# Optimization experiments

Hardware: AMD Instinct MI355X
Metric: run time of the kernel (lower is better)

The kernel has to match this reference:

```python
import jax, jax.numpy as jnp
import numpy as np

INV_L_MIN, INV_L_MAX = 0.5, 2.0

def _gelu(x):
    return jax.nn.gelu(x, approximate=False)

def _scaled_sigmoid(x, lo, hi):
    return lo + (hi - lo) * jax.nn.sigmoid(x)

def _fourier_bases(nodes, modes):
    # nodes: [b, n, d]; modes: [k, d, w] -> temp: [b, n, k, w]
    temp = 2.0 * jnp.pi * jnp.einsum('bxd,kdw->bxkw', nodes, modes)
    return jnp.cos(temp), jnp.sin(temp), jnp.ones_like(temp[:, :, :1, :])

def _spectral_conv(x, wc, ws, w0, bc, bs, b0, wbc, wbs, wb0):
    # x: [b, c_in, n]; forward non-uniform Fourier transform via weighted bases
    x_c = jnp.einsum('bix,bxkw->bikw', x, wbc)
    x_s = -jnp.einsum('bix,bxkw->bikw', x, wbs)
    x_0 = jnp.einsum('bix,bxkw->bikw', x, wb0)
    f_c = jnp.einsum('bikw,iokw->bokw', x_c, wc) - jnp.einsum('bikw,iokw->bokw', x_s, ws)
    f_s = jnp.einsum('bikw,iokw->bokw', x_s, wc) + jnp.einsum('bikw,iokw->bokw', x_c, ws)
    f_0 = jnp.einsum('bikw,iokw->bokw', x_0, w0)
    return (jnp.einsum('bokw,bxkw->box', f_0, b0)
            + 2.0 * jnp.einsum('bokw,bxkw->box', f_c, bc)
            - 2.0 * jnp.einsum('bokw,bxkw->box', f_s, bs))


def setup_inputs() -> dict:
    key = jax.random.key(0)
    ks = jax.random.split(key, 32)
    B, NU, NV = 4, 65536, 16384
    K, D, W = 32, 2, 1          # nmodes, ndims, nmeasures
    C, L = 64, 3                # channels, number of BNO layers
    FC, IU, IV, OUT = 128, 2, 3, 1
    f32 = jnp.float32
    rn = lambda k, s, sc=1.0: (sc * jax.random.normal(k, s, dtype=f32))
    ru = lambda k, s, sc=1.0: (sc * jax.random.uniform(k, s, dtype=f32))
    sp_scale = 1.0 / (C * C)
    inp = {
        'u': rn(ks[0], (B, NU, IU)),
        'v': rn(ks[1], (B, NV, IV)),
        'node_mask_u': jnp.ones((B, NU, 1), dtype=jnp.int32),
        'nodes_u': ru(ks[2], (B, NU, D)),
        'nodes_v': ru(ks[3], (B, NV, D)),
        'node_weights_u': ru(ks[4], (B, NU, W), 1.0 / NU),
        'node_weights_v': ru(ks[5], (B, NV, W), 1.0 / NV),
        'modes': ru(ks[6], (K, D, W), 8.0),
        # scaled_logit(1.0, 0.5, 2.0) = log((1-0.5)/(2-1)) = log(0.5)
        'inv_L_scale_latent': jnp.full((D, W), -0.69314718, dtype=f32),
        'fc0_u_w': rn(ks[7], (C, IU), 0.5), 'fc0_u_b': rn(ks[8], (C,), 0.1),
        'fc0_v_w': rn(ks[9], (C, IV), 0.5), 'fc0_v_b': rn(ks[10], (C,), 0.1),
        'sp_ext_wc': ru(ks[11], (L, C, C, K, W), sp_scale),
        'sp_ext_ws': ru(ks[12], (L, C, C, K, W), sp_scale),
        'sp_ext_w0': ru(ks[13], (L, C, C, 1, W), sp_scale),
        'sp_u_wc': ru(ks[14], (L, C, C, K, W), sp_scale),
        'sp_u_ws': ru(ks[15], (L, C, C, K, W), sp_scale),
        'sp_u_w0': ru(ks[16], (L, C, C, 1, W), sp_scale),
        'sp_v_wc': ru(ks[17], (L, C, C, K, W), sp_scale),
        'sp_v_ws': ru(ks[18], (L, C, C, K, W), sp_scale),
        'sp_v_w0': ru(ks[19], (L, C, C, 1, W), sp_scale),
        'ws_u_w': rn(ks[20], (L, C, C), 0.05), 'ws_u_b': rn(ks[21], (L, C), 0.02),
        'ws_v_w': rn(ks[22], (L, C, C), 0.05), 'ws_v_b': rn(ks[23], (L, C), 0.02),
        'fc1_w': rn(ks[24], (FC, C), 0.05), 'fc1_b': rn(ks[25], (FC,), 0.02),
        'fc2_w': rn(ks[26], (OUT, FC), 0.05), 'fc2_b': rn(ks[27], (OUT,), 0.02),
    }
    return inp


def reference(u, v, node_mask_u, nodes_u, nodes_v, node_weights_u, node_weights_v,
              modes, inv_L_scale_latent, fc0_u_w, fc0_u_b, fc0_v_w, fc0_v_b,
              sp_ext_wc, sp_ext_ws, sp_ext_w0, sp_u_wc, sp_u_ws, sp_u_w0,
              sp_v_wc, sp_v_ws, sp_v_w0, ws_u_w, ws_u_b, ws_v_w, ws_v_b,
              fc1_w, fc1_b, fc2_w, fc2_b):
    # node_mask_u is unpacked but unused in the original forward
    m = modes * _scaled_sigmoid(inv_L_scale_latent, INV_L_MIN, INV_L_MAX)  # [k,d,w]
    bc_u, bs_u, b0_u = _fourier_bases(nodes_u, m)
    bc_v, bs_v, b0_v = _fourier_bases(nodes_v, m)
    wu = node_weights_u[:, :, None, :]  # [b,x,1,w]
    wv = node_weights_v[:, :, None, :]
    wbc_u, wbs_u, wb0_u = bc_u * wu, bs_u * wu, b0_u * wu
    wbc_v, wbs_v, wb0_v = bc_v * wv, bs_v * wv, b0_v * wv
    # lift to channel dim and move to [b, c, n]
    u = jnp.einsum('bxi,oi->box', u, fc0_u_w) + fc0_u_b[None, :, None]
    v = jnp.einsum('bxi,oi->box', v, fc0_v_w) + fc0_v_b[None, :, None]
    L = ws_u_w.shape[0]
    for i in range(L):
        u1 = _spectral_conv(v, sp_ext_wc[i], sp_ext_ws[i], sp_ext_w0[i],
                            bc_u, bs_u, b0_u, wbc_v, wbs_v, wb0_v)
        u2 = _spectral_conv(u, sp_u_wc[i], sp_u_ws[i], sp_u_w0[i],
                            bc_u, bs_u, b0_u, wbc_u, wbs_u, wb0_u)
        u3 = jnp.einsum('oi,bix->box', ws_u_w[i], u) + ws_u_b[i][None, :, None]
        u = u1 + u2 + u3
        if i != L - 1:  # v is only updated on non-final layers, as in the original
            u = _gelu(u)
            v1 = _spectral_conv(v, sp_v_wc[i], sp_v_ws[i], sp_v_w0[i],
                                bc_v, bs_v, b0_v, wbc_v, wbs_v, wb0_v)
            v2 = jnp.einsum('oi,bix->box', ws_v_w[i], v) + ws_v_b[i][None, :, None]
            v = _gelu(v1 + v2)
    u = jnp.transpose(u, (0, 2, 1))  # [b, n, c]
    u = _gelu(u @ fc1_w.T + fc1_b)
    return u @ fc2_w.T + fc2_b
```

## Files before the change

kernel.cpp:

```cpp
#include <hip/hip_runtime.h>
#include <math.h>

#define PI2 6.283185307179586f

typedef __attribute__((ext_vector_type(8))) short bf16x8;
typedef __attribute__((ext_vector_type(4))) float f32x4;

__device__ __forceinline__ float gelu_f(float x) {
    return 0.5f * x * (1.0f + erff(x * 0.7071067811865476f));
}
__device__ __forceinline__ unsigned short f2bf(float f) {
    unsigned int u = __float_as_uint(f);
    u += 0x7FFFu + ((u >> 16) & 1u);
    return (unsigned short)(u >> 16);
}
__device__ __forceinline__ float bf2f(unsigned short h) {
    return __uint_as_float(((unsigned int)h) << 16);
}
__device__ __forceinline__ unsigned int pk(unsigned short a, unsigned short b) {
    return (unsigned int)a | ((unsigned int)b << 16);
}
__device__ __forceinline__ void wsplit(float w, unsigned short* dst) {
    unsigned short h = f2bf(w);
    dst[0] = h;
    dst[128] = f2bf(w - bf2f(h));
}

template<int NIN>
__global__ __launch_bounds__(256) void k_prep(const float* __restrict__ nodes, const float* __restrict__ modes,
                                              const float* __restrict__ latent, const float* __restrict__ nw,
                                              const float* __restrict__ inp, const float* __restrict__ fcw,
                                              const float* __restrict__ fcb,
                                              unsigned short* __restrict__ FT, unsigned short* __restrict__ wbb,
                                              unsigned short* __restrict__ chbf, int N) {
    int b = blockIdx.y;
    int x = blockIdx.x * 256 + threadIdx.x;
    float s0 = 0.5f + 1.5f / (1.0f + expf(-latent[0]));
    float s1 = 0.5f + 1.5f / (1.0f + expf(-latent[1]));
    float n0 = nodes[((size_t)b * N + x) * 2 + 0];
    float n1 = nodes[((size_t)b * N + x) * 2 + 1];
    float wx = nw[(size_t)b * N + x];
    unsigned short* wb = wbb + (size_t)b * 65 * N + x;
    unsigned int row[64];
    #pragma unroll
    for (int k = 0; k < 32; ++k) {
        float m0 = modes[k * 2 + 0] * s0;
        float m1 = modes[k * 2 + 1] * s1;
        float t = PI2 * (n0 * m0 + n1 * m1);
        float s, c;
        sincosf(t, &s, &c);
        unsigned short hc = f2bf(c), hs = f2bf(s);
        if (k & 1) { row[k >> 1] |= ((unsigned int)hc << 16); row[16 + (k >> 1)] |= ((unsigned int)hs << 16); }
        else       { row[k >> 1] = hc;                         row[16 + (k >> 1)] = hs; }
        wb[(size_t)k * N] = f2bf(c * wx);
        wb[(size_t)(32 + k) * N] = f2bf(s * wx);
    }
    wb[(size_t)64 * N] = f2bf(wx);
    float xi[NIN];
    #pragma unroll
    for (int i = 0; i < NIN; ++i) xi[i] = inp[((size_t)b * N + x) * NIN + i];
    unsigned short* cb = chbf + (size_t)b * 64 * N + x;
    #pragma unroll
    for (int c = 0; c < 64; ++c) {
        float a = fcb[c];
        #pragma unroll
        for (int i = 0; i < NIN; ++i) a += fcw[c * NIN + i] * xi[i];
        unsigned short h = f2bf(a);
        cb[(size_t)c * N] = h;
        if (c & 1) row[32 + (c >> 1)] |= ((unsigned int)h << 16);
        else row[32 + (c >> 1)] = h;
    }
    unsigned int* fr = (unsigned int*)(FT + ((size_t)b * N + x) * 128);
    #pragma unroll
    for (int i = 0; i < 64; ++i) fr[i] = row[i];
}

__global__ __launch_bounds__(256) void k_analysis2(const unsigned short* __restrict__ chbf_u,
                                                   const unsigned short* __restrict__ wbb_u,
                                                   const unsigned short* __restrict__ chbf_v,
                                                   const unsigned short* __restrict__ wbb_v,
                                                   float* __restrict__ part_u, float* __restrict__ part_v,
                                                   int NU_, int NV_, int chu, int chv) {
    int b = blockIdx.y, bx = blockIdx.x, tid = threadIdx.x;
    const unsigned short *chb, *wb;
    float* pb;
    int N, xlen, chunk;
    if (bx < chu) {
        chunk = bx; N = NU_; xlen = NU_ / chu;
        chb = chbf_u + (size_t)b * 64 * N;
        wb = wbb_u + (size_t)b * 65 * N;
        pb = part_u + (size_t)(b * chu + chunk) * 64 * 66;
    } else {
        chunk = bx - chu; N = NV_; xlen = NV_ / chv;
        chb = chbf_v + (size_t)b * 64 * N;
        wb = wbb_v + (size_t)b * 65 * N;
        pb = part_v + (size_t)(b * chv + chunk) * 64 * 66;
    }
    int lane = tid & 63, wv = tid >> 6;
    int lm = lane & 15, lg = lane >> 4;
    int ro = wv * 16;
    int x0 = chunk * xlen;
    f32x4 acc[5] = {};
    for (int x = x0; x < x0 + xlen; x += 32) {
        bf16x8 a = *(const bf16x8*)(chb + (size_t)(ro + lm) * N + x + lg * 8);
        #pragma unroll
        for (int ct = 0; ct < 4; ++ct) {
            bf16x8 bf = *(const bf16x8*)(wb + (size_t)(ct * 16 + lm) * N + x + lg * 8);
            acc[ct] = __builtin_amdgcn_mfma_f32_16x16x32_bf16(a, bf, acc[ct], 0, 0, 0);
        }
        bf16x8 wf = *(const bf16x8*)(wb + (size_t)64 * N + x + lg * 8);
        acc[4] = __builtin_amdgcn_mfma_f32_16x16x32_bf16(a, wf, acc[4], 0, 0, 0);
    }
    #pragma unroll
    for (int ct = 0; ct < 4; ++ct)
        #pragma unroll
        for (int j = 0; j < 4; ++j)
            pb[(ro + lg * 4 + j) * 66 + ct * 16 + lm] = acc[ct][j];
    if (lm == 0) {
        #pragma unroll
        for (int j = 0; j < 4; ++j) pb[(ro + lg * 4 + j) * 66 + 64] = acc[4][j];
    }
}

__global__ void k_reduce2(const float* __restrict__ part_u, const float* __restrict__ part_v,
                          float* __restrict__ momu, float* __restrict__ momv, int chu, int chv, int B_) {
    int by = blockIdx.y;
    const float* p;
    float* m;
    int nch, b;
    if (by < B_) { b = by; p = part_u; m = momu; nch = chu; }
    else { b = by - B_; p = part_v; m = momv; nch = chv; }
    int e = blockIdx.x * 256 + threadIdx.x;
    if (e >= 64 * 65) return;
    int row = e / 65, col = e % 65;
    const float* pp = p + ((size_t)(b * nch) * 64 + row) * 66 + col;
    float s = 0.f;
    #pragma unroll 4
    for (int c = 0; c < nch; ++c)
        s += pp[(size_t)c * 64 * 66];
    m[((size_t)b * 64 + row) * 66 + col] = s;
}

__global__ __launch_bounds__(256) void k_tw(const float* __restrict__ e_c, const float* __restrict__ e_s,
                                            const float* __restrict__ u_c, const float* __restrict__ u_s,
                                            const float* __restrict__ v_c, const float* __restrict__ v_s,
                                            float* __restrict__ oT) {
    int li = blockIdx.x;
    int a = blockIdx.y;
    const float* in;
    switch (a) {
        case 0: in = e_c; break;
        case 1: in = e_s; break;
        case 2: in = u_c; break;
        case 3: in = u_s; break;
        case 4: in = v_c; break;
        default: in = v_s; break;
    }
    float* outp = oT + (size_t)a * 393216;
    int l = li >> 6, i = li & 63;
    __shared__ float t[32][65];
    int tid = threadIdx.x;
    const float* ib = in + (size_t)l * 131072 + (size_t)i * 2048;
    #pragma unroll
    for (int r = 0; r < 8; ++r) {
        int e = r * 256 + tid;
        t[e & 31][e >> 5] = ib[e];
    }
    __syncthreads();
    float* ob = outp + (size_t)l * 131072 + (size_t)i * 64;
    #pragma unroll
    for (int r = 0; r < 8; ++r) {
        int e = r * 256 + tid;
        ob[(size_t)(e >> 6) * 4096 + (e & 63)] = t[e >> 6][e & 63];
    }
}

__global__ void k_buildW(const float* __restrict__ momu, const float* __restrict__ momv,
                         const float* __restrict__ ecT, const float* __restrict__ esT, const float* __restrict__ ew0,
                         const float* __restrict__ ucT, const float* __restrict__ usT, const float* __restrict__ uw0,
                         const float* __restrict__ vcT, const float* __restrict__ vsT, const float* __restrict__ vw0,
                         const float* __restrict__ wsuw, const float* __restrict__ wsub,
                         const float* __restrict__ wsvw, const float* __restrict__ wsvb,
                         unsigned short* __restrict__ WuBf, unsigned short* __restrict__ WvBf,
                         float* __restrict__ biasU, float* __restrict__ biasV, int do_v) {
    int b = blockIdx.y, j = blockIdx.x, o = threadIdx.x;
    const float* mu = momu + (size_t)b * 64 * 66;
    const float* mv = momv + (size_t)b * 64 * 66;
    unsigned short* Wub = WuBf + ((size_t)b * 64 + o) * 256;
    unsigned short* Wvb = WvBf + ((size_t)b * 64 + o) * 256;
    if (j < 32) {
        int k = j;
        const float* ec = ecT + (size_t)k * 4096;
        const float* es = esT + (size_t)k * 4096;
        const float* uc = ucT + (size_t)k * 4096;
        const float* us = usT + (size_t)k * 4096;
        const float* vc = vcT + (size_t)k * 4096;
        const float* vs = vsT + (size_t)k * 4096;
        float fcu = 0, fsu = 0, fcv = 0, fsv = 0;
        for (int i = 0; i < 64; ++i) {
            float Scv = mv[i * 66 + k], Ssv = mv[i * 66 + 32 + k];
            float Scu = mu[i * 66 + k], Ssu = mu[i * 66 + 32 + k];
            int wi = i * 64 + o;
            float e_c = ec[wi], e_s = es[wi];
            float u_c = uc[wi], u_s = us[wi];
            fcu += Scv * e_c + Ssv * e_s + Scu * u_c + Ssu * u_s;
            fsu += Scv * e_s - Ssv * e_c + Scu * u_s - Ssu * u_c;
            if (do_v) {
                float v_c = vc[wi], v_s = vs[wi];
                fcv += Scv * v_c + Ssv * v_s;
                fsv += Scv * v_s - Ssv * v_c;
            }
        }
        wsplit(2.f * fcu, Wub + k);
        wsplit(-2.f * fsu, Wub + 32 + k);
        if (do_v) {
            wsplit(2.f * fcv, Wvb + k);
            wsplit(-2.f * fsv, Wvb + 32 + k);
        }
    } else {
        for (int c = 0; c < 64; ++c) wsplit(wsuw[o * 64 + c], Wub + 64 + c);
        float f0u = 0;
        for (int i = 0; i < 64; ++i)
            f0u += mv[i * 66 + 64] * ew0[i * 64 + o] + mu[i * 66 + 64] * uw0[i * 64 + o];
        biasU[b * 64 + o] = f0u + wsub[o];
        if (do_v) {
            for (int c = 0; c < 64; ++c) wsplit(wsvw[o * 64 + c], Wvb + 64 + c);
            float f0v = 0;
            for (int i = 0; i < 64; ++i) f0v += mv[i * 66 + 64] * vw0[i * 64 + o];
            biasV[b * 64 + o] = f0v + wsvb[o];
        }
    }
}

__global__ void k_buildW_slow(const float* __restrict__ momu, const float* __restrict__ momv,
                              const float* __restrict__ ewc, const float* __restrict__ ews, const float* __restrict__ ew0,
                              const float* __restrict__ uwc, const float* __restrict__ uws, const float* __restrict__ uw0,
                              const float* __restrict__ vwc, const float* __restrict__ vws, const float* __restrict__ vw0,
                              const float* __restrict__ wsuw, const float* __restrict__ wsub,
                              const float* __restrict__ wsvw, const float* __restrict__ wsvb,
                              unsigned short* __restrict__ WuBf, unsigned short* __restrict__ WvBf,
                              float* __restrict__ biasU, float* __restrict__ biasV, int do_v) {
    int b = blockIdx.y, j = blockIdx.x, o = threadIdx.x;
    const float* mu = momu + (size_t)b * 64 * 66;
    const float* mv = momv + (size_t)b * 64 * 66;
    unsigned short* Wub = WuBf + ((size_t)b * 64 + o) * 256;
    unsigned short* Wvb = WvBf + ((size_t)b * 64 + o) * 256;
    if (j < 32) {
        int k = j;
        float fcu = 0, fsu = 0, fcv = 0, fsv = 0;
        for (int i = 0; i < 64; ++i) {
            float Scv = mv[i * 66 + k], Ssv = mv[i * 66 + 32 + k];
            float Scu = mu[i * 66 + k], Ssu = mu[i * 66 + 32 + k];
            int wi = (i * 64 + o) * 32 + k;
            float ec = ewc[wi], es = ews[wi];
            float uc = uwc[wi], us = uws[wi];
            fcu += Scv * ec + Ssv * es + Scu * uc + Ssu * us;
            fsu += Scv * es - Ssv * ec + Scu * us - Ssu * uc;
            if (do_v) {
                float vc = vwc[wi], vs = vws[wi];
                fcv += Scv * vc + Ssv * vs;
                fsv += Scv * vs - Ssv * vc;
            }
        }
        wsplit(2.f * fcu, Wub + k);
        wsplit(-2.f * fsu, Wub + 32 + k);
        if (do_v) {
            wsplit(2.f * fcv, Wvb + k);
            wsplit(-2.f * fsv, Wvb + 32 + k);
        }
    } else {
        for (int c = 0; c < 64; ++c) wsplit(wsuw[o * 64 + c], Wub + 64 + c);
        float f0u = 0;
        for (int i = 0; i < 64; ++i)
            f0u += mv[i * 66 + 64] * ew0[i * 64 + o] + mu[i * 66 + 64] * uw0[i * 64 + o];
        biasU[b * 64 + o] = f0u + wsub[o];
        if (do_v) {
            for (int c = 0; c < 64; ++c) wsplit(wsvw[o * 64 + c], Wvb + 64 + c);
            float f0v = 0;
            for (int i = 0; i < 64; ++i) f0v += mv[i * 66 + 64] * vw0[i * 64 + o];
            biasV[b * 64 + o] = f0v + wsvb[o];
        }
    }
}

__global__ __launch_bounds__(256) void k_synth3(const unsigned short* __restrict__ WuBf,
                                                const unsigned short* __restrict__ WvBf,
                                                const float* __restrict__ biasU, const float* __restrict__ biasV,
                                                unsigned short* FTu, unsigned short* FTv,
                                                const unsigned short* __restrict__ wbb_u,
                                                const unsigned short* __restrict__ wbb_v,
                                                float* __restrict__ part_u, float* __restrict__ part_v,
                                                int NU_, int NV_, int nbu, int act_u, int wft_v, int do_mom) {
    int bx = blockIdx.x, b = blockIdx.y, tid = threadIdx.x;
    const unsigned short* Wb;
    const float* bi;
    unsigned short* FT;
    const unsigned short* wb;
    float* pb;
    int N, act, wft, blk;
    if (bx < nbu) {
        blk = bx; Wb = WuBf; bi = biasU; FT = FTu; N = NU_;
        wb = wbb_u + (size_t)b * 65 * NU_;
        pb = part_u + (size_t)(b * (NU_ / 256) + blk) * 64 * 66;
        act = act_u; wft = 1;
    } else {
        blk = bx - nbu; Wb = WvBf; bi = biasV; FT = FTv; N = NV_;
        wb = wbb_v + (size_t)b * 65 * NV_;
        pb = part_v + (size_t)(b * (NV_ / 256) + blk) * 64 * 66;
        act = 1; wft = wft_v;
    }
    int lane = tid & 63, wv = tid >> 6;
    int lm = lane & 15, lg = lane >> 4;
    int ro = wv * 16;
    const unsigned short* Wrow = Wb + ((size_t)b * 64 + ro + lm) * 256;
    bf16x8 ahi[4], alo[4];
    #pragma unroll
    for (int kt = 0; kt < 4; ++kt) {
        ahi[kt] = *(const bf16x8*)(Wrow + kt * 32 + lg * 8);
        alo[kt] = *(const bf16x8*)(Wrow + 128 + kt * 32 + lg * 8);
    }
    float bias[4];
    #pragma unroll
    for (int j = 0; j < 4; ++j) bias[j] = bi[b * 64 + ro + lg * 4 + j];
    unsigned short* ftb = FT + (size_t)b * N * 128;
    __shared__ unsigned short st2[64][136];
    f32x4 macc[5] = {};
    int r0 = ro + lg * 4;
    for (int t = 0; t < 2; ++t) {
        int x0 = blk * 256 + t * 128;
        f32x4 acc[8] = {};
        #pragma unroll
        for (int xt = 0; xt < 8; ++xt) {
            int x = x0 + xt * 16 + lm;
            const unsigned short* fp = ftb + (size_t)x * 128 + lg * 8;
            #pragma unroll
            for (int kt = 0; kt < 4; ++kt) {
                bf16x8 bf = *(const bf16x8*)(fp + kt * 32);
                acc[xt] = __builtin_amdgcn_mfma_f32_16x16x32_bf16(ahi[kt], bf, acc[xt], 0, 0, 0);
                acc[xt] = __builtin_amdgcn_mfma_f32_16x16x32_bf16(alo[kt], bf, acc[xt], 0, 0, 0);
            }
        }
        __syncthreads();
        #pragma unroll
        for (int xt = 0; xt < 8; ++xt) {
            int xl = xt * 16 + lm;
            float v[4];
            #pragma unroll
            for (int j = 0; j < 4; ++j) {
                v[j] = acc[xt][j] + bias[j];
                if (act) v[j] = gelu_f(v[j]);
            }
            unsigned short h[4];
            #pragma unroll
            for (int j = 0; j < 4; ++j) h[j] = f2bf(v[j]);
            if (do_mom) {
                st2[r0 + 0][xl] = h[0];
                st2[r0 + 1][xl] = h[1];
                st2[r0 + 2][xl] = h[2];
                st2[r0 + 3][xl] = h[3];
            }
            if (wft) {
                unsigned int* dst = (unsigned int*)(ftb + (size_t)(x0 + xl) * 128 + 64 + r0);
                dst[0] = pk(h[0], h[1]);
                dst[1] = pk(h[2], h[3]);
            }
        }
        if (do_mom) {
            __syncthreads();
            #pragma unroll
            for (int xs = 0; xs < 128; xs += 32) {
                bf16x8 a = *(const bf16x8*)&st2[ro + lm][xs + lg * 8];
                #pragma unroll
                for (int ct = 0; ct < 4; ++ct) {
                    bf16x8 bw = *(const bf16x8*)(wb + (size_t)(ct * 16 + lm) * N + x0 + xs + lg * 8);
                    macc[ct] = __builtin_amdgcn_mfma_f32_16x16x32_bf16(a, bw, macc[ct], 0, 0, 0);
                }
                bf16x8 wf = *(const bf16x8*)(wb + (size_t)64 * N + x0 + xs + lg * 8);
                macc[4] = __builtin_amdgcn_mfma_f32_16x16x32_bf16(a, wf, macc[4], 0, 0, 0);
            }
        }
    }
    if (do_mom) {
        #pragma unroll
        for (int ct = 0; ct < 4; ++ct)
            #pragma unroll
            for (int j = 0; j < 4; ++j)
                pb[(r0 + j) * 66 + ct * 16 + lm] = macc[ct][j];
        if (lm == 0) {
            #pragma unroll
            for (int j = 0; j < 4; ++j) pb[(r0 + j) * 66 + 64] = macc[4][j];
        }
    }
}

__global__ __launch_bounds__(256) void k_fc12(const unsigned short* __restrict__ FT, const float* __restrict__ w1,
                                              const float* __restrict__ b1, const float* __restrict__ w2,
                                              const float* __restrict__ b2, float* __restrict__ out, int N) {
    int b = blockIdx.y, blk = blockIdx.x, tid = threadIdx.x;
    int lane = tid & 63, wv = tid >> 6;
    int lm = lane & 15, lg = lane >> 4;
    int f0 = wv * 32;
    bf16x8 ahi[2][2], alo[2][2];
    #pragma unroll
    for (int ft = 0; ft < 2; ++ft)
        #pragma unroll
        for (int kt = 0; kt < 2; ++kt) {
            const float* wp = w1 + (size_t)(f0 + ft * 16 + lm) * 64 + kt * 32 + lg * 8;
            float tmp[8];
            *(float4*)&tmp[0] = *(const float4*)wp;
            *(float4*)&tmp[4] = *(const float4*)(wp + 4);
            #pragma unroll
            for (int i = 0; i < 8; ++i) {
                unsigned short h = f2bf(tmp[i]);
                ahi[ft][kt][i] = (short)h;
                alo[ft][kt][i] = (short)f2bf(tmp[i] - bf2f(h));
            }
        }
    float b1v[2][4], w2v[2][4];
    #pragma unroll
    for (int ft = 0; ft < 2; ++ft)
        #pragma unroll
        for (int j = 0; j < 4; ++j) {
            int f = f0 + ft * 16 + lg * 4 + j;
            b1v[ft][j] = b1[f];
            w2v[ft][j] = w2[f];
        }
    f32x4 acc[8][2] = {};
    const unsigned short* ftb = FT + (size_t)b * N * 128;
    int x0 = blk * 128;
    #pragma unroll
    for (int xt = 0; xt < 8; ++xt) {
        const unsigned short* fp = ftb + (size_t)(x0 + xt * 16 + lm) * 128 + 64 + lg * 8;
        bf16x8 bf0 = *(const bf16x8*)fp;
        bf16x8 bf1 = *(const bf16x8*)(fp + 32);
        #pragma unroll
        for (int ft = 0; ft < 2; ++ft) {
            acc[xt][ft] = __builtin_amdgcn_mfma_f32_16x16x32_bf16(ahi[ft][0], bf0, acc[xt][ft], 0, 0, 0);
            acc[xt][ft] = __builtin_amdgcn_mfma_f32_16x16x32_bf16(alo[ft][0], bf0, acc[xt][ft], 0, 0, 0);
            acc[xt][ft] = __builtin_amdgcn_mfma_f32_16x16x32_bf16(ahi[ft][1], bf1, acc[xt][ft], 0, 0, 0);
            acc[xt][ft] = __builtin_amdgcn_mfma_f32_16x16x32_bf16(alo[ft][1], bf1, acc[xt][ft], 0, 0, 0);
        }
    }
    __shared__ float red[4][8][16];
    #pragma unroll
    for (int xt = 0; xt < 8; ++xt) {
        float s = 0.f;
        #pragma unroll
        for (int ft = 0; ft < 2; ++ft)
            #pragma unroll
            for (int j = 0; j < 4; ++j) {
                float v = acc[xt][ft][j] + b1v[ft][j];
                s += w2v[ft][j] * gelu_f(v);
            }
        s += __shfl_xor(s, 16, 64);
        s += __shfl_xor(s, 32, 64);
        if (lg == 0) red[wv][xt][lm] = s;
    }
    __syncthreads();
    if (tid < 128) {
        int xt = tid >> 4, lmm = tid & 15;
        float s = b2[0] + red[0][xt][lmm] + red[1][xt][lmm] + red[2][xt][lmm] + red[3][xt][lmm];
        out[(size_t)b * N + x0 + tid] = s;
    }
}

extern "C" void kernel_launch(void* const* d_in, const int* in_sizes, int n_in,
                              void* d_out, int out_size, void* d_ws, size_t ws_size,
                              hipStream_t stream) {
    const float* u_in = (const float*)d_in[0];
    const float* v_in = (const float*)d_in[1];
    const float* nodes_u = (const float*)d_in[3];
    const float* nodes_v = (const float*)d_in[4];
    const float* nwu = (const float*)d_in[5];
    const float* nwv = (const float*)d_in[6];
    const float* modes = (const float*)d_in[7];
    const float* latent = (const float*)d_in[8];
    const float* fc0uw = (const float*)d_in[9];
    const float* fc0ub = (const float*)d_in[10];
    const float* fc0vw = (const float*)d_in[11];
    const float* fc0vb = (const float*)d_in[12];
    const float* ewc = (const float*)d_in[13];
    const float* ews = (const float*)d_in[14];
    const float* ew0 = (const float*)d_in[15];
    const float* uwc = (const float*)d_in[16];
    const float* uws = (const float*)d_in[17];
    const float* uw0 = (const float*)d_in[18];
    const float* vwc = (const float*)d_in[19];
    const float* vws = (const float*)d_in[20];
    const float* vw0 = (const float*)d_in[21];
    const float* wsuw = (const float*)d_in[22];
    const float* wsub = (const float*)d_in[23];
    const float* wsvw = (const float*)d_in[24];
    const float* wsvb = (const float*)d_in[25];
    const float* fc1w = (const float*)d_in[26];
    const float* fc1b = (const float*)d_in[27];
    const float* fc2w = (const float*)d_in[28];
    const float* fc2b = (const float*)d_in[29];
    float* out = (float*)d_out;

    const int B = 4, NU = 65536, NV = 16384;
    const int CH_U = 256, CH_V = 128;

    unsigned short* FT_u = (unsigned short*)d_ws;
    unsigned short* FT_v = FT_u + (size_t)B * NU * 128;
    unsigned short* wbb_u = FT_v + (size_t)B * NV * 128;
    unsigned short* wbb_v = wbb_u + (size_t)B * 65 * NU;
    unsigned short* chbf_u = wbb_v + (size_t)B * 65 * NV;
    unsigned short* chbf_v = chbf_u + (size_t)B * 64 * NU;
    float* part_u = (float*)(chbf_v + (size_t)B * 64 * NV);
    float* part_v = part_u + (size_t)B * CH_U * 64 * 66;
    float* momu = part_v + (size_t)B * CH_V * 64 * 66;
    float* momv = momu + B * 64 * 66;
    unsigned short* WuBf = (unsigned short*)(momv + B * 64 * 66);
    unsigned short* WvBf = WuBf + (size_t)B * 64 * 256;
    float* biasU = (float*)(WvBf + (size_t)B * 64 * 256);
    float* biasV = biasU + B * 64;
    float* wT = biasV + B * 64;
    size_t need_T = (size_t)((char*)(wT + 6 * 393216) - (char*)d_ws);
    int use_T = (ws_size >= need_T) ? 1 : 0;

    k_prep<2><<<dim3(NU / 256, B), 256, 0, stream>>>(nodes_u, modes, latent, nwu, u_in, fc0uw, fc0ub,
                                                     FT_u, wbb_u, chbf_u, NU);
    k_prep<3><<<dim3(NV / 256, B), 256, 0, stream>>>(nodes_v, modes, latent, nwv, v_in, fc0vw, fc0vb,
                                                     FT_v, wbb_v, chbf_v, NV);
    if (use_T)
        k_tw<<<dim3(192, 6), 256, 0, stream>>>(ewc, ews, uwc, uws, vwc, vws, wT);

    k_analysis2<<<dim3(CH_U + CH_V, B), 256, 0, stream>>>(chbf_u, wbb_u, chbf_v, wbb_v,
                                                          part_u, part_v, NU, NV, CH_U, CH_V);

    for (int l = 0; l < 3; ++l) {
        int do_v = (l < 2) ? 1 : 0;
        int chu_l = (l == 0) ? CH_U : NU / 256;
        int chv_l = (l == 0) ? CH_V : NV / 256;
        k_reduce2<<<dim3(17, 2 * B), 256, 0, stream>>>(part_u, part_v, momu, momv, chu_l, chv_l, B);
        if (use_T) {
            k_buildW<<<dim3(33, B), 64, 0, stream>>>(momu, momv,
                wT + 0 * 393216 + l * 131072, wT + 1 * 393216 + l * 131072, ew0 + (size_t)l * 64 * 64,
                wT + 2 * 393216 + l * 131072, wT + 3 * 393216 + l * 131072, uw0 + (size_t)l * 64 * 64,
                wT + 4 * 393216 + l * 131072, wT + 5 * 393216 + l * 131072, vw0 + (size_t)l * 64 * 64,
                wsuw + l * 64 * 64, wsub + l * 64, wsvw + l * 64 * 64, wsvb + l * 64,
                WuBf, WvBf, biasU, biasV, do_v);
        } else {
            k_buildW_slow<<<dim3(33, B), 64, 0, stream>>>(momu, momv,
                ewc + (size_t)l * 64 * 64 * 32, ews + (size_t)l * 64 * 64 * 32, ew0 + (size_t)l * 64 * 64,
                uwc + (size_t)l * 64 * 64 * 32, uws + (size_t)l * 64 * 64 * 32, uw0 + (size_t)l * 64 * 64,
                vwc + (size_t)l * 64 * 64 * 32, vws + (size_t)l * 64 * 64 * 32, vw0 + (size_t)l * 64 * 64,
                wsuw + l * 64 * 64, wsub + l * 64, wsvw + l * 64 * 64, wsvb + l * 64,
                WuBf, WvBf, biasU, biasV, do_v);
        }
        int nbu2 = NU / 256;
        int nbx = nbu2 + (do_v ? NV / 256 : 0);
        int do_mom = (l < 2) ? 1 : 0;
        int wft_v = (l == 0) ? 1 : 0;
        k_synth3<<<dim3(nbx, B), 256, 0, stream>>>(WuBf, WvBf, biasU, biasV, FT_u, FT_v,
                                                   wbb_u, wbb_v, part_u, part_v,
                                                   NU, NV, nbu2, do_v , wft_v, do_mom);
    }
    k_fc12<<<dim3(NU / 128, B), 256, 0, stream>>>(FT_u, fc1w, fc1b, fc2w, fc2b, out, NU);
}
```

Before: 525.6 us.

## Halve synth block width, double grid, and parallelise partial-moment reduction

k_synth3 now handles 128 nodes per block instead of 256, so it launches twice as many blocks and each block writes its own partial-moment tile. The larger partial buffers are placed in reused workspace (the chbf_u region and slotA). k_reduce2 now splits each output element's channel sum across 8 threads and combines them through shared memory, with more blocks in the grid. The aim is better occupancy and latency hiding, at the cost of twice the partial-moment traffic and reuse of workspace that must no longer be live.

Result: faster. 504.8 us (-4.0%).

```diff
diff --git a/kernel.cpp b/kernel.cpp
--- a/kernel.cpp
+++ b/kernel.cpp
@@ -122,23 +122,35 @@
     }
 }
 
-__global__ void k_reduce2(const float* __restrict__ part_u, const float* __restrict__ part_v,
-                          float* __restrict__ momu, float* __restrict__ momv, int chu, int chv, int B_) {
+__global__ __launch_bounds__(256) void k_reduce2(const float* __restrict__ part_u, const float* __restrict__ part_v,
+                                                 float* __restrict__ momu, float* __restrict__ momv,
+                                                 int chu, int chv, int B_) {
     int by = blockIdx.y;
     const float* p;
     float* m;
     int nch, b;
     if (by < B_) { b = by; p = part_u; m = momu; nch = chu; }
     else { b = by - B_; p = part_v; m = momv; nch = chv; }
-    int e = blockIdx.x * 256 + threadIdx.x;
-    if (e >= 64 * 65) return;
-    int row = e / 65, col = e % 65;
-    const float* pp = p + ((size_t)(b * nch) * 64 + row) * 66 + col;
+    int eg = threadIdx.x >> 3;
+    int sp = threadIdx.x & 7;
+    int e = blockIdx.x * 32 + eg;
+    __shared__ float red[32][8];
     float s = 0.f;
-    #pragma unroll 4
-    for (int c = 0; c < nch; ++c)
-        s += pp[(size_t)c * 64 * 66];
-    m[((size_t)b * 64 + row) * 66 + col] = s;
+    int row = 0, col = 0;
+    if (e < 64 * 65) {
+        row = e / 65; col = e % 65;
+        const float* pp = p + ((size_t)(b * nch) * 64 + row) * 66 + col;
+        for (int c = sp; c < nch; c += 8)
+            s += pp[(size_t)c * 64 * 66];
+    }
+    red[eg][sp] = s;
+    __syncthreads();
+    if (sp == 0 && e < 64 * 65) {
+        float t = 0.f;
+        #pragma unroll
+        for (int i = 0; i < 8; ++i) t += red[eg][i];
+        m[((size_t)b * 64 + row) * 66 + col] = t;
+    }
 }
 
 __global__ __launch_bounds__(256) void k_tw(const float* __restrict__ e_c, const float* __restrict__ e_s,
@@ -301,12 +313,12 @@
     if (bx < nbu) {
         blk = bx; Wb = WuBf; bi = biasU; FT = FTu; N = NU_;
         wb = wbb_u + (size_t)b * 65 * NU_;
-        pb = part_u + (size_t)(b * (NU_ / 256) + blk) * 64 * 66;
+        pb = part_u + (size_t)(b * (NU_ / 128) + blk) * 64 * 66;
         act = act_u; wft = 1;
     } else {
         blk = bx - nbu; Wb = WvBf; bi = biasV; FT = FTv; N = NV_;
         wb = wbb_v + (size_t)b * 65 * NV_;
-        pb = part_v + (size_t)(b * (NV_ / 256) + blk) * 64 * 66;
+        pb = part_v + (size_t)(b * (NV_ / 128) + blk) * 64 * 66;
         act = 1; wft = wft_v;
     }
     int lane = tid & 63, wv = tid >> 6;
@@ -324,63 +336,59 @@
     for (int j = 0; j < 4; ++j) bias[j] = bi[b * 64 + ro + lg * 4 + j];
     unsigned short* ftb = FT + (size_t)b * N * 128;
     __shared__ unsigned short st2[64][136];
-    f32x4 macc[5] = {};
     int r0 = ro + lg * 4;
-    for (int t = 0; t < 2; ++t) {
-        int x0 = blk * 256 + t * 128;
-        f32x4 acc[8] = {};
-        #pragma unroll
-        for (int xt = 0; xt < 8; ++xt) {
-            int x = x0 + xt * 16 + lm;
-            const unsigned short* fp = ftb + (size_t)x * 128 + lg * 8;
+    int x0 = blk * 128;
+    f32x4 acc[8] = {};
+    #pragma unroll
+    for (int xt = 0; xt < 8; ++xt) {
+        int x = x0 + xt * 16 + lm;
+        const unsigned short* fp = ftb + (size_t)x * 128 + lg * 8;
+        #pragma unroll
+        for (int kt = 0; kt < 4; ++kt) {
+            bf16x8 bf = *(const bf16x8*)(fp + kt * 32);
+            acc[xt] = __builtin_amdgcn_mfma_f32_16x16x32_bf16(ahi[kt], bf, acc[xt], 0, 0, 0);
+            acc[xt] = __builtin_amdgcn_mfma_f32_16x16x32_bf16(alo[kt], bf, acc[xt], 0, 0, 0);
+        }
+    }
+    __syncthreads();
+    #pragma unroll
+    for (int xt = 0; xt < 8; ++xt) {
+        int xl = xt * 16 + lm;
+        float v[4];
+        #pragma unroll
+        for (int j = 0; j < 4; ++j) {
+            v[j] = acc[xt][j] + bias[j];
+            if (act) v[j] = gelu_f(v[j]);
+        }
+        unsigned short h[4];
+        #pragma unroll
+        for (int j = 0; j < 4; ++j) h[j] = f2bf(v[j]);
+        if (do_mom) {
+            st2[r0 + 0][xl] = h[0];
+            st2[r0 + 1][xl] = h[1];
+            st2[r0 + 2][xl] = h[2];
+            st2[r0 + 3][xl] = h[3];
+        }
+        if (wft) {
+            unsigned int* dst = (unsigned int*)(ftb + (size_t)(x0 + xl) * 128 + 64 + r0);
+            dst[0] = pk(h[0], h[1]);
+            dst[1] = pk(h[2], h[3]);
+        }
+    }
+    if (do_mom) {
+        __syncthreads();
+        f32x4 macc[5] = {};
+        #pragma unroll
+        for (int xs = 0; xs < 128; xs += 32) {
+            bf16x8 a = *(const bf16x8*)&st2[ro + lm][xs + lg * 8];
             #pragma unroll
-            for (int kt = 0; kt < 4; ++kt) {
-                bf16x8 bf = *(const bf16x8*)(fp + kt * 32);
-                acc[xt] = __builtin_amdgcn_mfma_f32_16x16x32_bf16(ahi[kt], bf, acc[xt], 0, 0, 0);
-                acc[xt] = __builtin_amdgcn_mfma_f32_16x16x32_bf16(alo[kt], bf, acc[xt], 0, 0, 0);
+            for (int ct = 0; ct < 4; ++ct) {
+                bf16x8 bw = *(const bf16x8*)(wb + (size_t)(ct * 16 + lm) * N + x0 + xs + lg * 8);
+                macc[ct] = __builtin_amdgcn_mfma_f32_16x16x32_bf16(a, bw, macc[ct], 0, 0, 0);
             }
-        }
-        __syncthreads();
-        #pragma unroll
-        for (int xt = 0; xt < 8; ++xt) {
-            int xl = xt * 16 + lm;
-            float v[4];
-            #pragma unroll
-            for (int j = 0; j < 4; ++j) {
-                v[j] = acc[xt][j] + bias[j];
-                if (act) v[j] = gelu_f(v[j]);
-            }
-            unsigned short h[4];
-            #pragma unroll
-            for (int j = 0; j < 4; ++j) h[j] = f2bf(v[j]);
-            if (do_mom) {
-                st2[r0 + 0][xl] = h[0];
-                st2[r0 + 1][xl] = h[1];
-                st2[r0 + 2][xl] = h[2];
-                st2[r0 + 3][xl] = h[3];
-            }
-            if (wft) {
-                unsigned int* dst = (unsigned int*)(ftb + (size_t)(x0 + xl) * 128 + 64 + r0);
-                dst[0] = pk(h[0], h[1]);
-                dst[1] = pk(h[2], h[3]);
-            }
-        }
-        if (do_mom) {
-            __syncthreads();
-            #pragma unroll
-            for (int xs = 0; xs < 128; xs += 32) {
-                bf16x8 a = *(const bf16x8*)&st2[ro + lm][xs + lg * 8];
-                #pragma unroll
-                for (int ct = 0; ct < 4; ++ct) {
-                    bf16x8 bw = *(const bf16x8*)(wb + (size_t)(ct * 16 + lm) * N + x0 + xs + lg * 8);
-                    macc[ct] = __builtin_amdgcn_mfma_f32_16x16x32_bf16(a, bw, macc[ct], 0, 0, 0);
-                }
-                bf16x8 wf = *(const bf16x8*)(wb + (size_t)64 * N + x0 + xs + lg * 8);
-                macc[4] = __builtin_amdgcn_mfma_f32_16x16x32_bf16(a, wf, macc[4], 0, 0, 0);
-            }
-        }
-    }
-    if (do_mom) {
+            bf16x8 wf = *(const bf16x8*)(wb + (size_t)64 * N + x0 + xs + lg * 8);
+            macc[4] = __builtin_amdgcn_mfma_f32_16x16x32_bf16(a, wf, macc[4], 0, 0, 0);
+        }
         #pragma unroll
         for (int ct = 0; ct < 4; ++ct)
             #pragma unroll
@@ -499,7 +507,8 @@
     float* out = (float*)d_out;
 
     const int B = 4, NU = 65536, NV = 16384;
-    const int CH_U = 256, CH_V = 128;
+    const int CH_U0 = 256, CH_V0 = 128;
+    const int CH_UL = NU / 128, CH_VL = NV / 128;
 
     unsigned short* FT_u = (unsigned short*)d_ws;
     unsigned short* FT_v = FT_u + (size_t)B * NU * 128;
@@ -507,9 +516,9 @@
     unsigned short* wbb_v = wbb_u + (size_t)B * 65 * NU;
     unsigned short* chbf_u = wbb_v + (size_t)B * 65 * NV;
     unsigned short* chbf_v = chbf_u + (size_t)B * 64 * NU;
-    float* part_u = (float*)(chbf_v + (size_t)B * 64 * NV);
-    float* part_v = part_u + (size_t)B * CH_U * 64 * 66;
-    float* momu = part_v + (size_t)B * CH_V * 64 * 66;
+    float* slotA = (float*)(chbf_v + (size_t)B * 64 * NV);
+    float* slotB = slotA + (size_t)B * CH_U0 * 64 * 66;
+    float* momu = slotB + (size_t)B * CH_V0 * 64 * 66;
     float* momv = momu + B * 64 * 66;
     unsigned short* WuBf = (unsigned short*)(momv + B * 64 * 66);
     unsigned short* WvBf = WuBf + (size_t)B * 64 * 256;
@@ -519,6 +528,11 @@
     size_t need_T = (size_t)((char*)(wT + 6 * 393216) - (char*)d_ws);
     int use_T = (ws_size >= need_T) ? 1 : 0;
 
+    float* part0_u = slotA;
+    float* part0_v = slotB;
+    float* partL_u = (float*)chbf_u;
+    float* partL_v = slotA;
+
     k_prep<2><<<dim3(NU / 256, B), 256, 0, stream>>>(nodes_u, modes, latent, nwu, u_in, fc0uw, fc0ub,
                                                      FT_u, wbb_u, chbf_u, NU);
     k_prep<3><<<dim3(NV / 256, B), 256, 0, stream>>>(nodes_v, modes, latent, nwv, v_in, fc0vw, fc0vb,
@@ -526,14 +540,16 @@
     if (use_T)
         k_tw<<<dim3(192, 6), 256, 0, stream>>>(ewc, ews, uwc, uws, vwc, vws, wT);
 
-    k_analysis2<<<dim3(CH_U + CH_V, B), 256, 0, stream>>>(chbf_u, wbb_u, chbf_v, wbb_v,
-                                                          part_u, part_v, NU, NV, CH_U, CH_V);
+    k_analysis2<<<dim3(CH_U0 + CH_V0, B), 256, 0, stream>>>(chbf_u, wbb_u, chbf_v, wbb_v,
+                                                            part0_u, part0_v, NU, NV, CH_U0, CH_V0);
 
     for (int l = 0; l < 3; ++l) {
         int do_v = (l < 2) ? 1 : 0;
-        int chu_l = (l == 0) ? CH_U : NU / 256;
-        int chv_l = (l == 0) ? CH_V : NV / 256;
-        k_reduce2<<<dim3(17, 2 * B), 256, 0, stream>>>(part_u, part_v, momu, momv, chu_l, chv_l, B);
+        const float* ru = (l == 0) ? part0_u : partL_u;
+        const float* rv = (l == 0) ? part0_v : partL_v;
+        int chu_l = (l == 0) ? CH_U0 : CH_UL;
+        int chv_l = (l == 0) ? CH_V0 : CH_VL;
+        k_reduce2<<<dim3(130, 2 * B), 256, 0, stream>>>(ru, rv, momu, momv, chu_l, chv_l, B);
         if (use_T) {
             k_buildW<<<dim3(33, B), 64, 0, stream>>>(momu, momv,
                 wT + 0 * 393216 + l * 131072, wT + 1 * 393216 + l * 131072, ew0 + (size_t)l * 64 * 64,
@@ -549,13 +565,13 @@
                 wsuw + l * 64 * 64, wsub + l * 64, wsvw + l * 64 * 64, wsvb + l * 64,
                 WuBf, WvBf, biasU, biasV, do_v);
         }
-        int nbu2 = NU / 256;
-        int nbx = nbu2 + (do_v ? NV / 256 : 0);
+        int nbu = NU / 128;
+        int nbx = nbu + (do_v ? NV / 128 : 0);
         int do_mom = (l < 2) ? 1 : 0;
         int wft_v = (l == 0) ? 1 : 0;
         k_synth3<<<dim3(nbx, B), 256, 0, stream>>>(WuBf, WvBf, biasU, biasV, FT_u, FT_v,
-                                                   wbb_u, wbb_v, part_u, part_v,
-                                                   NU, NV, nbu2, do_v , wft_v, do_mom);
+                                                   wbb_u, wbb_v, partL_u, partL_v,
+                                                   NU, NV, nbu, do_v , wft_v, do_mom);
     }
     k_fc12<<<dim3(NU / 128, B), 256, 0, stream>>>(FT_u, fc1w, fc1b, fc2w, fc2b, out, NU);
 }
```
